# Kernel optimization log

Hardware: AMD Instinct MI355X
Metric: run time of the kernel (lower is better)

## Reference

```python
import jax, jax.numpy as jnp
import numpy as np

# Module hyperparameters (init_kwargs)
NFILT = 128          # args.filter_num
FILTER_SIZE = 1025   # args.filter_size
NFFT = 2048          # args.NFFT
SIGMA_COFF = 0.02    # args.sigma_coff
F = NFFT // 2 + 1                    # 1025 frequency bins
HALF = (NFFT // 2 + 1) // NFILT // 4  # half filter length = 2

B, T = 32, 3000


def setup_inputs() -> dict:
    key = jax.random.key(0)
    k1, k2, k3 = jax.random.split(key, 3)
    inputs = jax.random.normal(k1, (B, F, T), dtype=jnp.float32)
    # 'random' initializer: cn = 1/nfilt, sigma = sigma_coff (+ tiny noise)
    cn = jnp.full((NFILT,), 1.0 / NFILT, jnp.float32) + 5e-4 * jax.random.normal(k2, (NFILT,), jnp.float32)
    sigma = jnp.full((NFILT,), SIGMA_COFF, jnp.float32) + 1e-3 * jax.random.normal(k3, (NFILT,), jnp.float32)
    w = jnp.stack([cn, sigma], axis=1)  # [nfilt, 2]
    return {"inputs": inputs, "w": w}


def make_fbanks(cn, sigma):
    # clamps as in gaussianFreqFilters
    sigma = jnp.clip(sigma, 1e-4, 0.05)
    cn = jnp.clip(cn, 30.0 / 80000.0, 1.0)
    c = jnp.cumsum(cn)                                   # [nfilt] centers (fraction)
    ic = jnp.floor(c * FILTER_SIZE).astype(jnp.int32)    # int(center_Location)
    lo = ic - HALF
    band_low = jnp.where((lo >= 0) & (lo < FILTER_SIZE), lo, 0)
    hi = ic + HALF
    band_high = jnp.where(hi < FILTER_SIZE, hi + 1, FILTER_SIZE - 1)
    j = jnp.arange(F)
    t = j.astype(cn.dtype) / FILTER_SIZE                 # [F]
    z = (t[None, :] - c[:, None]) / sigma[:, None]       # [nfilt, F]
    g = jnp.exp(-0.5 * z * z)
    mask = (j[None, :] >= band_low[:, None]) & (j[None, :] < band_high[:, None])
    return jnp.where(mask, g, jnp.zeros((), g.dtype))    # [nfilt, F]


def param_dis_cum(x):
    s = jnp.sum(x)
    loss = jnp.where(s < 0.2, jnp.exp(-s), jnp.exp(s)) * 100.0
    return jnp.where((s >= 0.2) & (s <= 0.5), jnp.zeros((), x.dtype), loss)


def param_less_zero(x):
    return jnp.sum(jnp.where(x < 0, -x, jnp.zeros((), x.dtype))) * 1000.0


def reference(inputs, w):
    cn = w[:, 0]
    sigma = w[:, 1]
    filters = make_fbanks(cn, sigma)                 # [nfilt, F]
    # inputs.permute(0,2,1) @ filters.T -> permute back: [B, nfilt, T]
    res = jnp.einsum('bft,nf->bnt', inputs, filters)
    loss = param_less_zero(cn) + param_dis_cum(cn) + param_less_zero(sigma)
    return res, loss
```

## Files before the change

kernel.cpp:

```cpp
#include <hip/hip_runtime.h>
#include <hip/hip_bf16.h>
#include <math.h>

constexpr int NFILT = 128;
constexpr int FILTER_SIZE = 1025;
constexpr int HALF = 2;
constexpr int F_DIM = 1025;
constexpr int B_DIM = 32;
constexpr int T_DIM = 3000;

constexpr int NCHUNK = 16;
constexpr int NPC = NFILT / NCHUNK;
constexpr int MAXW = 8;

__global__ __launch_bounds__(128) void gauss_setup(
    const float* __restrict__ w,
    float* __restrict__ c_out,
    float* __restrict__ rsg_out,
    int* __restrict__ lo_out,
    int* __restrict__ wd_out,
    float* __restrict__ wt_out,
    float* __restrict__ loss_out) {
    __shared__ float cn_sh[NFILT];
    __shared__ float sg_sh[NFILT];
    __shared__ float c_sh[NFILT];
    const int tid = threadIdx.x;

    cn_sh[tid] = w[2 * tid];
    sg_sh[tid] = w[2 * tid + 1];
    __syncthreads();

    if (tid == 0) {
        float c = 0.0f;
        float s_cn = 0.0f, pl_cn = 0.0f, pl_sig = 0.0f;
        for (int i = 0; i < NFILT; ++i) {
            float cn = cn_sh[i];
            float sg = sg_sh[i];
            s_cn += cn;
            if (cn < 0.0f) pl_cn += -cn;
            if (sg < 0.0f) pl_sig += -sg;
            float cnc = cn;
            if (cnc < 30.0f / 80000.0f) cnc = 30.0f / 80000.0f;
            if (cnc > 1.0f) cnc = 1.0f;
            c += cnc;
            c_sh[i] = c;
        }
        float loss = (pl_cn + pl_sig) * 1000.0f;
        float pdc;
        if (s_cn >= 0.2f && s_cn <= 0.5f) pdc = 0.0f;
        else pdc = (s_cn < 0.2f ? expf(-s_cn) : expf(s_cn)) * 100.0f;
        loss_out[0] = loss + pdc;
    }
    __syncthreads();

    float sg = sg_sh[tid];
    if (sg < 0.0001f) sg = 0.0001f;
    if (sg > 0.05f) sg = 0.05f;
    const float c = c_sh[tid];

    int ic = (int)floorf(c * (float)FILTER_SIZE);
    int lo = ic - HALF;
    int blo = (lo >= 0 && lo < FILTER_SIZE) ? lo : 0;
    int hi = ic + HALF;
    int bhi = (hi < FILTER_SIZE) ? (hi + 1) : (FILTER_SIZE - 1);
    int wd = bhi - blo;
    if (wd < 0) wd = 0;

    c_out[tid] = c;
    rsg_out[tid] = 1.0f / sg;
    lo_out[tid] = blo;
    wd_out[tid] = wd;

    for (int j = 0; j < MAXW; ++j) {
        float g = 0.0f;
        if (j < wd) {
            float tv = (float)(blo + j) / (float)FILTER_SIZE;
            float z = (tv - c) / sg;
            g = expf(-0.5f * z * z);
        }
        wt_out[tid * MAXW + j] = g;
    }
}

__global__ __launch_bounds__(256) void gauss_apply(
    const float* __restrict__ in,
    const float* __restrict__ cArr,
    const float* __restrict__ rsgArr,
    const int* __restrict__ loArr,
    const int* __restrict__ wdArr,
    const float* __restrict__ wtArr,
    float* __restrict__ out) {
    __shared__ float c_sh[NPC], rsg_sh[NPC];
    __shared__ int lo_sh[NPC], wd_sh[NPC];
    __shared__ float wt_sh[NPC][MAXW];

    const int tid = threadIdx.x;
    const int chunk = blockIdx.y;
    const int b = blockIdx.z;
    const int n0 = chunk * NPC;

    if (tid < NPC) {
        c_sh[tid] = cArr[n0 + tid];
        rsg_sh[tid] = rsgArr[n0 + tid];
        lo_sh[tid] = loArr[n0 + tid];
        wd_sh[tid] = wdArr[n0 + tid];
    }
    if (tid < NPC * MAXW) {
        wt_sh[tid / MAXW][tid % MAXW] = wtArr[n0 * MAXW + tid];
    }
    __syncthreads();

    const int t0 = blockIdx.x * 1024 + tid * 4;
    if (t0 >= T_DIM) return;

    const float* inb = in + (size_t)b * F_DIM * T_DIM;
    float* outb = out + ((size_t)b * NFILT + (size_t)n0) * T_DIM;

    for (int ni = 0; ni < NPC; ++ni) {
        const int lo = lo_sh[ni];
        const int wd = wd_sh[ni];
        const float* src = inb + (size_t)lo * T_DIM + t0;

        float ax = 0.0f, ay = 0.0f, az = 0.0f, aw = 0.0f;
        if (wd == 5) {
            #pragma unroll
            for (int j = 0; j < 5; ++j) {
                const float g = wt_sh[ni][j];
                const float4 v = *reinterpret_cast<const float4*>(src + (size_t)j * T_DIM);
                ax += g * v.x; ay += g * v.y; az += g * v.z; aw += g * v.w;
            }
        } else if (wd <= MAXW) {
            for (int j = 0; j < wd; ++j) {
                const float g = wt_sh[ni][j];
                const float4 v = *reinterpret_cast<const float4*>(src + (size_t)j * T_DIM);
                ax += g * v.x; ay += g * v.y; az += g * v.z; aw += g * v.w;
            }
        } else {
            const float c = c_sh[ni];
            const float rsg = rsg_sh[ni];
            for (int j = 0; j < wd; ++j) {
                float tv = (float)(lo + j) / (float)FILTER_SIZE;
                float z = (tv - c) * rsg;
                float g = expf(-0.5f * z * z);
                const float4 v = *reinterpret_cast<const float4*>(src + (size_t)j * T_DIM);
                ax += g * v.x; ay += g * v.y; az += g * v.z; aw += g * v.w;
            }
        }
        float4 r; r.x = ax; r.y = ay; r.z = az; r.w = aw;
        *reinterpret_cast<float4*>(outb + (size_t)ni * T_DIM + t0) = r;
    }
}

extern "C" void kernel_launch(void* const* d_in, const int* in_sizes, int n_in,
                              void* d_out, int out_size, void* d_ws, size_t ws_size,
                              hipStream_t stream) {
    const float* inputs = (const float*)d_in[0];
    const float* w = (const float*)d_in[1];

    float* out = (float*)d_out;
    float* loss_out = out + (size_t)B_DIM * NFILT * T_DIM;

    float* c_arr = (float*)d_ws;
    float* rsg_arr = c_arr + NFILT;
    int* lo_arr = (int*)(rsg_arr + NFILT);
    int* wd_arr = lo_arr + NFILT;
    float* wt_arr = (float*)(wd_arr + NFILT);

    gauss_setup<<<1, 128, 0, stream>>>(w, c_arr, rsg_arr, lo_arr, wd_arr,
                                       wt_arr, loss_out);

    dim3 grid((T_DIM + 1023) / 1024, NCHUNK, B_DIM);
    gauss_apply<<<grid, 256, 0, stream>>>(inputs, c_arr, rsg_arr, lo_arr,
                                          wd_arr, wt_arr, out);
}
```

Measured before the change: 57.58 us.

## Fuse filter setup into apply kernel and use nontemporal output stores

Removes the separate single-block setup kernel: each block of the apply kernel now computes the cumulative filter centers, band limits and Gaussian weights for its own chunk in shared memory, and one designated block writes the loss. This drops a kernel launch and the serial dependency between the two kernels. In exchange, every block redoes a 128-step serial prefix sum on one thread before it can start loading data. Output stores are also switched to nontemporal vector stores so the streaming writes bypass cache retention.

```diff
diff --git a/kernel.cpp b/kernel.cpp
--- a/kernel.cpp
+++ b/kernel.cpp
@@ -1,5 +1,4 @@
 #include <hip/hip_runtime.h>
-#include <hip/hip_bf16.h>
 #include <math.h>
 
 constexpr int NFILT = 128;
@@ -13,84 +12,15 @@
 constexpr int NPC = NFILT / NCHUNK;
 constexpr int MAXW = 8;
 
-__global__ __launch_bounds__(128) void gauss_setup(
+typedef float f32x4 __attribute__((ext_vector_type(4)));
+
+__global__ __launch_bounds__(256) void gauss_fused(
     const float* __restrict__ w,
-    float* __restrict__ c_out,
-    float* __restrict__ rsg_out,
-    int* __restrict__ lo_out,
-    int* __restrict__ wd_out,
-    float* __restrict__ wt_out,
+    const float* __restrict__ in,
+    float* __restrict__ out,
     float* __restrict__ loss_out) {
-    __shared__ float cn_sh[NFILT];
-    __shared__ float sg_sh[NFILT];
-    __shared__ float c_sh[NFILT];
-    const int tid = threadIdx.x;
-
-    cn_sh[tid] = w[2 * tid];
-    sg_sh[tid] = w[2 * tid + 1];
-    __syncthreads();
-
-    if (tid == 0) {
-        float c = 0.0f;
-        float s_cn = 0.0f, pl_cn = 0.0f, pl_sig = 0.0f;
-        for (int i = 0; i < NFILT; ++i) {
-            float cn = cn_sh[i];
-            float sg = sg_sh[i];
-            s_cn += cn;
-            if (cn < 0.0f) pl_cn += -cn;
-            if (sg < 0.0f) pl_sig += -sg;
-            float cnc = cn;
-            if (cnc < 30.0f / 80000.0f) cnc = 30.0f / 80000.0f;
-            if (cnc > 1.0f) cnc = 1.0f;
-            c += cnc;
-            c_sh[i] = c;
-        }
-        float loss = (pl_cn + pl_sig) * 1000.0f;
-        float pdc;
-        if (s_cn >= 0.2f && s_cn <= 0.5f) pdc = 0.0f;
-        else pdc = (s_cn < 0.2f ? expf(-s_cn) : expf(s_cn)) * 100.0f;
-        loss_out[0] = loss + pdc;
-    }
-    __syncthreads();
-
-    float sg = sg_sh[tid];
-    if (sg < 0.0001f) sg = 0.0001f;
-    if (sg > 0.05f) sg = 0.05f;
-    const float c = c_sh[tid];
-
-    int ic = (int)floorf(c * (float)FILTER_SIZE);
-    int lo = ic - HALF;
-    int blo = (lo >= 0 && lo < FILTER_SIZE) ? lo : 0;
-    int hi = ic + HALF;
-    int bhi = (hi < FILTER_SIZE) ? (hi + 1) : (FILTER_SIZE - 1);
-    int wd = bhi - blo;
-    if (wd < 0) wd = 0;
-
-    c_out[tid] = c;
-    rsg_out[tid] = 1.0f / sg;
-    lo_out[tid] = blo;
-    wd_out[tid] = wd;
-
-    for (int j = 0; j < MAXW; ++j) {
-        float g = 0.0f;
-        if (j < wd) {
-            float tv = (float)(blo + j) / (float)FILTER_SIZE;
-            float z = (tv - c) / sg;
-            g = expf(-0.5f * z * z);
-        }
-        wt_out[tid * MAXW + j] = g;
-    }
-}
-
-__global__ __launch_bounds__(256) void gauss_apply(
-    const float* __restrict__ in,
-    const float* __restrict__ cArr,
-    const float* __restrict__ rsgArr,
-    const int* __restrict__ loArr,
-    const int* __restrict__ wdArr,
-    const float* __restrict__ wtArr,
-    float* __restrict__ out) {
-    __shared__ float c_sh[NPC], rsg_sh[NPC];
+    __shared__ float cn_sh[NFILT], sg_sh[NFILT], c_sh[NFILT];
+    __shared__ float cc_sh[NPC], rsg_sh[NPC];
     __shared__ int lo_sh[NPC], wd_sh[NPC];
     __shared__ float wt_sh[NPC][MAXW];
 
@@ -99,14 +29,70 @@
     const int b = blockIdx.z;
     const int n0 = chunk * NPC;
 
+    if (tid < NFILT) cn_sh[tid] = w[2 * tid];
+    else             sg_sh[tid - NFILT] = w[2 * (tid - NFILT) + 1];
+    __syncthreads();
+
+    if (tid == 0) {
+        float c = 0.0f;
+        for (int i = 0; i < NFILT; ++i) {
+            float cnc = cn_sh[i];
+            if (cnc < 30.0f / 80000.0f) cnc = 30.0f / 80000.0f;
+            if (cnc > 1.0f) cnc = 1.0f;
+            c += cnc;
+            c_sh[i] = c;
+        }
+    }
+    if (tid == 64 && blockIdx.x == 0 && chunk == 0 && b == 0) {
+        float s_cn = 0.0f, pl = 0.0f;
+        for (int i = 0; i < NFILT; ++i) {
+            float cn = cn_sh[i];
+            float sg = sg_sh[i];
+            s_cn += cn;
+            if (cn < 0.0f) pl += -cn;
+            if (sg < 0.0f) pl += -sg;
+        }
+        float loss = pl * 1000.0f;
+        float pdc;
+        if (s_cn >= 0.2f && s_cn <= 0.5f) pdc = 0.0f;
+        else pdc = (s_cn < 0.2f ? expf(-s_cn) : expf(s_cn)) * 100.0f;
+        loss_out[0] = loss + pdc;
+    }
+    __syncthreads();
+
     if (tid < NPC) {
-        c_sh[tid] = cArr[n0 + tid];
-        rsg_sh[tid] = rsgArr[n0 + tid];
-        lo_sh[tid] = loArr[n0 + tid];
-        wd_sh[tid] = wdArr[n0 + tid];
+        const int n = n0 + tid;
+        const float c = c_sh[n];
+        float sg = sg_sh[n];
+        if (sg < 0.0001f) sg = 0.0001f;
+        if (sg > 0.05f) sg = 0.05f;
+        int ic = (int)floorf(c * (float)FILTER_SIZE);
+        int lo = ic - HALF;
+        int blo = (lo >= 0 && lo < FILTER_SIZE) ? lo : 0;
+        int hi = ic + HALF;
+        int bhi = (hi < FILTER_SIZE) ? (hi + 1) : (FILTER_SIZE - 1);
+        int wd = bhi - blo;
+        if (wd < 0) wd = 0;
+        cc_sh[tid] = c;
+        rsg_sh[tid] = 1.0f / sg;
+        lo_sh[tid] = blo;
+        wd_sh[tid] = wd;
     }
+    __syncthreads();
+
     if (tid < NPC * MAXW) {
-        wt_sh[tid / MAXW][tid % MAXW] = wtArr[n0 * MAXW + tid];
+        const int ni = tid / MAXW, j = tid % MAXW;
+        float g = 0.0f;
+        if (j < wd_sh[ni]) {
+            const int n = n0 + ni;
+            float sg = sg_sh[n];
+            if (sg < 0.0001f) sg = 0.0001f;
+            if (sg > 0.05f) sg = 0.05f;
+            float tv = (float)(lo_sh[ni] + j) / (float)FILTER_SIZE;
+            float z = (tv - cc_sh[ni]) / sg;
+            g = expf(-0.5f * z * z);
+        }
+        wt_sh[ni][j] = g;
     }
     __syncthreads();
 
@@ -126,28 +112,30 @@
             #pragma unroll
             for (int j = 0; j < 5; ++j) {
                 const float g = wt_sh[ni][j];
-                const float4 v = *reinterpret_cast<const float4*>(src + (size_t)j * T_DIM);
+                const f32x4 v = *reinterpret_cast<const f32x4*>(src + (size_t)j * T_DIM);
                 ax += g * v.x; ay += g * v.y; az += g * v.z; aw += g * v.w;
             }
         } else if (wd <= MAXW) {
             for (int j = 0; j < wd; ++j) {
                 const float g = wt_sh[ni][j];
-                const float4 v = *reinterpret_cast<const float4*>(src + (size_t)j * T_DIM);
+                const f32x4 v = *reinterpret_cast<const f32x4*>(src + (size_t)j * T_DIM);
                 ax += g * v.x; ay += g * v.y; az += g * v.z; aw += g * v.w;
             }
         } else {
-            const float c = c_sh[ni];
+            const float c = cc_sh[ni];
             const float rsg = rsg_sh[ni];
             for (int j = 0; j < wd; ++j) {
                 float tv = (float)(lo + j) / (float)FILTER_SIZE;
                 float z = (tv - c) * rsg;
                 float g = expf(-0.5f * z * z);
-                const float4 v = *reinterpret_cast<const float4*>(src + (size_t)j * T_DIM);
+                const f32x4 v = *reinterpret_cast<const f32x4*>(src + (size_t)j * T_DIM);
                 ax += g * v.x; ay += g * v.y; az += g * v.z; aw += g * v.w;
             }
         }
-        float4 r; r.x = ax; r.y = ay; r.z = az; r.w = aw;
-        *reinterpret_cast<float4*>(outb + (size_t)ni * T_DIM + t0) = r;
+        f32x4 r;
+        r.x = ax; r.y = ay; r.z = az; r.w = aw;
+        __builtin_nontemporal_store(
+            r, reinterpret_cast<f32x4*>(outb + (size_t)ni * T_DIM + t0));
     }
 }
 
@@ -160,16 +148,6 @@
     float* out = (float*)d_out;
     float* loss_out = out + (size_t)B_DIM * NFILT * T_DIM;
 
-    float* c_arr = (float*)d_ws;
-    float* rsg_arr = c_arr + NFILT;
-    int* lo_arr = (int*)(rsg_arr + NFILT);
-    int* wd_arr = lo_arr + NFILT;
-    float* wt_arr = (float*)(wd_arr + NFILT);
-
-    gauss_setup<<<1, 128, 0, stream>>>(w, c_arr, rsg_arr, lo_arr, wd_arr,
-                                       wt_arr, loss_out);
-
     dim3 grid((T_DIM + 1023) / 1024, NCHUNK, B_DIM);
-    gauss_apply<<<grid, 256, 0, stream>>>(inputs, c_arr, rsg_arr, lo_arr,
-                                          wd_arr, wt_arr, out);
+    gauss_fused<<<grid, 256, 0, stream>>>(w, inputs, out, loss_out);
 }
```

Measured after the change: 58.53 us. No clear change (+1.6%).

## Cover full time row per block, double filter chunks, use nontemporal stores

Applied to the files above, without the earlier changes.

Each block now handles an entire 3000-sample row: every thread processes three float4 columns, with the last column clamped and its store masked. This replaces the old grid of three time-tiles per block, most of which left threads idle in the last tile. Filter chunks double from 16 to 32, so each block handles 4 filters and the grid becomes 1x32x32. Output writes use nontemporal stores so they do not pollute the cache. In exchange, each thread carries more accumulator registers and there are fewer blocks in total.

```diff
diff --git a/kernel.cpp b/kernel.cpp
--- a/kernel.cpp
+++ b/kernel.cpp
@@ -1,5 +1,4 @@
 #include <hip/hip_runtime.h>
-#include <hip/hip_bf16.h>
 #include <math.h>
 
 constexpr int NFILT = 128;
@@ -9,9 +8,12 @@
 constexpr int B_DIM = 32;
 constexpr int T_DIM = 3000;
 
-constexpr int NCHUNK = 16;
+constexpr int NCHUNK = 32;
 constexpr int NPC = NFILT / NCHUNK;
 constexpr int MAXW = 8;
+constexpr int NF4 = T_DIM / 4;
+
+typedef float f32x4 __attribute__((ext_vector_type(4)));
 
 __global__ __launch_bounds__(128) void gauss_setup(
     const float* __restrict__ w,
@@ -110,8 +112,10 @@
     }
     __syncthreads();
 
-    const int t0 = blockIdx.x * 1024 + tid * 4;
-    if (t0 >= T_DIM) return;
+    const int f40 = tid;
+    const int f41 = tid + 256;
+    const bool ok2 = (tid + 512) < NF4;
+    const int f42 = ok2 ? (tid + 512) : (NF4 - 1);
 
     const float* inb = in + (size_t)b * F_DIM * T_DIM;
     float* outb = out + ((size_t)b * NFILT + (size_t)n0) * T_DIM;
@@ -119,35 +123,52 @@
     for (int ni = 0; ni < NPC; ++ni) {
         const int lo = lo_sh[ni];
         const int wd = wd_sh[ni];
-        const float* src = inb + (size_t)lo * T_DIM + t0;
+        const float* src = inb + (size_t)lo * T_DIM;
 
-        float ax = 0.0f, ay = 0.0f, az = 0.0f, aw = 0.0f;
+        f32x4 a0 = {0.f, 0.f, 0.f, 0.f};
+        f32x4 a1 = {0.f, 0.f, 0.f, 0.f};
+        f32x4 a2 = {0.f, 0.f, 0.f, 0.f};
+
         if (wd == 5) {
             #pragma unroll
-            for (int j = 0; j < 5; ++j) {
-                const float g = wt_sh[ni][j];
-                const float4 v = *reinterpret_cast<const float4*>(src + (size_t)j * T_DIM);
-                ax += g * v.x; ay += g * v.y; az += g * v.z; aw += g * v.w;
+            for (int r = 0; r < 5; ++r) {
+                const float g = wt_sh[ni][r];
+                const float* row = src + (size_t)r * T_DIM;
+                const f32x4 v0 = *reinterpret_cast<const f32x4*>(row + 4 * (size_t)f40);
+                const f32x4 v1 = *reinterpret_cast<const f32x4*>(row + 4 * (size_t)f41);
+                const f32x4 v2 = *reinterpret_cast<const f32x4*>(row + 4 * (size_t)f42);
+                a0 += g * v0; a1 += g * v1; a2 += g * v2;
             }
         } else if (wd <= MAXW) {
-            for (int j = 0; j < wd; ++j) {
-                const float g = wt_sh[ni][j];
-                const float4 v = *reinterpret_cast<const float4*>(src + (size_t)j * T_DIM);
-                ax += g * v.x; ay += g * v.y; az += g * v.z; aw += g * v.w;
+            for (int r = 0; r < wd; ++r) {
+                const float g = wt_sh[ni][r];
+                const float* row = src + (size_t)r * T_DIM;
+                const f32x4 v0 = *reinterpret_cast<const f32x4*>(row + 4 * (size_t)f40);
+                const f32x4 v1 = *reinterpret_cast<const f32x4*>(row + 4 * (size_t)f41);
+                const f32x4 v2 = *reinterpret_cast<const f32x4*>(row + 4 * (size_t)f42);
+                a0 += g * v0; a1 += g * v1; a2 += g * v2;
             }
         } else {
             const float c = c_sh[ni];
             const float rsg = rsg_sh[ni];
-            for (int j = 0; j < wd; ++j) {
-                float tv = (float)(lo + j) / (float)FILTER_SIZE;
+            for (int r = 0; r < wd; ++r) {
+                float tv = (float)(lo + r) / (float)FILTER_SIZE;
                 float z = (tv - c) * rsg;
                 float g = expf(-0.5f * z * z);
-                const float4 v = *reinterpret_cast<const float4*>(src + (size_t)j * T_DIM);
-                ax += g * v.x; ay += g * v.y; az += g * v.z; aw += g * v.w;
+                const float* row = src + (size_t)r * T_DIM;
+                const f32x4 v0 = *reinterpret_cast<const f32x4*>(row + 4 * (size_t)f40);
+                const f32x4 v1 = *reinterpret_cast<const f32x4*>(row + 4 * (size_t)f41);
+                const f32x4 v2 = *reinterpret_cast<const f32x4*>(row + 4 * (size_t)f42);
+                a0 += g * v0; a1 += g * v1; a2 += g * v2;
             }
         }
-        float4 r; r.x = ax; r.y = ay; r.z = az; r.w = aw;
-        *reinterpret_cast<float4*>(outb + (size_t)ni * T_DIM + t0) = r;
+
+        float* orow = outb + (size_t)ni * T_DIM;
+        __builtin_nontemporal_store(a0, reinterpret_cast<f32x4*>(orow + 4 * (size_t)f40));
+        __builtin_nontemporal_store(a1, reinterpret_cast<f32x4*>(orow + 4 * (size_t)f41));
+        if (ok2) {
+            __builtin_nontemporal_store(a2, reinterpret_cast<f32x4*>(orow + 4 * (size_t)f42));
+        }
     }
 }
 
@@ -169,7 +190,7 @@
     gauss_setup<<<1, 128, 0, stream>>>(w, c_arr, rsg_arr, lo_arr, wd_arr,
                                        wt_arr, loss_out);
 
-    dim3 grid((T_DIM + 1023) / 1024, NCHUNK, B_DIM);
+    dim3 grid(1, NCHUNK, B_DIM);
     gauss_apply<<<grid, 256, 0, stream>>>(inputs, c_arr, rsg_arr, lo_arr,
                                           wd_arr, wt_arr, out);
 }
```

New measurement: 55.59 us. 1.04x faster.
